# Optimization experiments

Measured on AMD Instinct MI355X. Metric: run time of the kernel, lower is better.

## Reference

```python
import jax, jax.numpy as jnp
import numpy as np

B, T = 32, 128
D_PATCH, D_PLM, H, P = 128, 768, 4, 64
HD = D_PLM // H          # head_dim = 192
N_TOK = 15               # 1+1+4+4+4+1 patch tokens
EPS = 1e-5


def layernorm(x, g, b):
    m = jnp.mean(x, axis=-1, keepdims=True)
    v = jnp.var(x, axis=-1, keepdims=True)
    return (x - m) * jax.lax.rsqrt(v + EPS) * g + b


def setup_inputs() -> dict:
    key = jax.random.key(0)
    ks = jax.random.split(key, 12)
    nrm = lambda k, shp, s: jax.random.normal(k, shp, jnp.float32) * s
    return {
        "state":    jax.random.normal(ks[0], (B, T, 6, 6), jnp.float32),
        # per-feature patch embedders: scalar feats (0,1,5) in_dim=1, windowed feats (2,3,4) in_dim=3
        "w_scalar": nrm(ks[1], (3, 1, D_PATCH), 0.5),
        "b_scalar": jnp.zeros((3, D_PATCH), jnp.float32),
        "w_patch":  nrm(ks[2], (3, 3, D_PATCH), 0.3),
        "b_patch":  jnp.zeros((3, D_PATCH), jnp.float32),
        "feat_emb": nrm(ks[3], (6, D_PATCH), 0.02),
        "pn_g": jnp.ones((D_PATCH,), jnp.float32),
        "pn_b": jnp.zeros((D_PATCH,), jnp.float32),
        "wq": nrm(ks[4], (D_PATCH, D_PLM), 0.05), "bq": jnp.zeros((D_PLM,), jnp.float32),
        "wk": nrm(ks[5], (D_PLM, D_PLM), 0.02),   "bk": jnp.zeros((D_PLM,), jnp.float32),
        "wv": nrm(ks[6], (D_PLM, D_PLM), 0.02),   "bv": jnp.zeros((D_PLM,), jnp.float32),
        "wp": nrm(ks[7], (D_PATCH, D_PLM), 0.05), "bp": jnp.zeros((D_PLM,), jnp.float32),
        "wo": nrm(ks[8], (D_PLM, D_PLM), 0.02),   "bo": jnp.zeros((D_PLM,), jnp.float32),
        "on_g": jnp.ones((D_PLM,), jnp.float32),
        "on_b": jnp.zeros((D_PLM,), jnp.float32),
        # text prototype bank (rows sampled from word embedding table in the original)
        "protos": nrm(ks[9], (P, D_PLM), 1.0),
    }


def reference(state, w_scalar, b_scalar, w_patch, b_patch, feat_emb, pn_g, pn_b,
              wq, bq, wk, bk, wv, bv, wp, bp, wo, bo, on_g, on_b, protos):
    b, t = state.shape[0], state.shape[1]
    s = state.reshape(b * t, 6, 6)                       # (N,6,6)
    N = s.shape[0]

    # scalar features 0,1,5: last timestep, patch_size=1 -> 1 token each
    sc = s[:, jnp.array([0, 1, 5]), -1]                  # (N,3)
    sc_emb = sc[..., None] * w_scalar[:, 0][None] + b_scalar[None]   # (N,3,Dp)
    sc_emb = sc_emb + feat_emb[jnp.array([0, 1, 5])][None]

    # windowed features 2,3,4: length 6, patch_len 3, stride 1 -> 4 tokens each
    pf = s[:, jnp.array([2, 3, 4]), :]                   # (N,3,6)
    win = jnp.stack([pf[..., i:i + 3] for i in range(4)], axis=2)    # (N,3,4,3)
    p_emb = jnp.einsum('nfkp,fpd->nfkd', win, w_patch) + b_patch[None, :, None]
    p_emb = p_emb + feat_emb[jnp.array([2, 3, 4])][None, :, None]

    # concat in feature order 0,1,2,3,4,5 -> (N,15,Dp), then LayerNorm
    pe = jnp.concatenate([sc_emb[:, 0:1], sc_emb[:, 1:2],
                          p_emb[:, 0], p_emb[:, 1], p_emb[:, 2],
                          sc_emb[:, 2:3]], axis=1)
    pe = layernorm(pe, pn_g, pn_b)

    # cross-attention: Q from patches, K/V from 64 text prototypes
    q = (pe @ wq + bq).reshape(N, N_TOK, H, HD)
    k = (protos @ wk + bk).reshape(P, H, HD)
    v = (protos @ wv + bv).reshape(P, H, HD)
    scores = jnp.einsum('nthd,phd->nhtp', q, k) / np.float32(np.sqrt(HD))
    attn = jax.nn.softmax(scores, axis=-1)               # (N,H,T,P)
    rep = jnp.einsum('nhtp,phd->nthd', attn, v).reshape(N, N_TOK, D_PLM)

    out = (rep @ wo + bo) + (pe @ wp + bp)               # dual projection residual
    out = layernorm(out, on_g, on_b)
    return out.reshape(b, t, N_TOK, D_PLM)
```

## Files before the change

### kernel.cpp

```cpp
#include <hip/hip_runtime.h>

#define NTOK 15
#define DP   128
#define DM   768
#define NH   4
#define HD   192
#define NP   64
#define EPSF 1e-5f
#define RPB  4
#define TPB  512
#define KW   384

typedef __attribute__((ext_vector_type(8))) short bf16x8;
typedef __attribute__((ext_vector_type(4))) float f32x4;

__device__ __forceinline__ unsigned short f2bf(float x) {
    unsigned u = __float_as_uint(x);
    u = (u + 0x7FFF + ((u >> 16) & 1)) >> 16;
    return (unsigned short)u;
}
__device__ __forceinline__ int swzP(int row, int b) { return row * 256 + (b ^ ((row & 7) << 4)); }
__device__ __forceinline__ int swzB(int row, int b) { return row * 512 + (b ^ ((row & 7) << 4)); }

__global__ __launch_bounds__(768) void kv_kernel(
    const float* __restrict__ protos,
    const float* __restrict__ wk, const float* __restrict__ bk,
    const float* __restrict__ wv, const float* __restrict__ bv,
    float* __restrict__ Kraw, float* __restrict__ Vf)
{
    int r = blockIdx.x;
    int j = threadIdx.x;
    __shared__ float prow[DM];
    prow[j] = protos[r * DM + j];
    __syncthreads();
    float aK = bk[j], aV = bv[j];
    for (int d = 0; d < DM; ++d) {
        float p = prow[d];
        aK += p * wk[d * DM + j];
        aV += p * wv[d * DM + j];
    }
    int h = j / HD, jj = j - h * HD;
    Kraw[(h * NP + r) * HD + jj] = aK;
    Vf[r * DM + j] = aV;
}

__global__ __launch_bounds__(256) void fold_kernel(
    const float* __restrict__ Kraw, const float* __restrict__ Vf,
    const float* __restrict__ wq, const float* __restrict__ bq,
    const float* __restrict__ wo, const float* __restrict__ wp,
    unsigned short* __restrict__ KWb, float* __restrict__ kqb,
    unsigned short* __restrict__ Wcat)
{
    int b = blockIdx.x, tid = threadIdx.x;
    if (b >= 256) {
        int idx = (b - 256) * 256 + tid;
        int j = idx >> 7, d = idx & 127;
        Wcat[(size_t)j * KW + 256 + d] = f2bf(wp[d * DM + j]);
        return;
    }
    int hp = b, h = hp >> 6, p = hp & 63;
    __shared__ float Kl[HD], Vl[HD];
    if (tid < HD) {
        Kl[tid] = Kraw[hp * HD + tid];
        Vl[tid] = Vf[p * DM + h * HD + tid];
    }
    __syncthreads();
    const float scale = 0.07216878364870323f;
    if (tid < DP) {
        float a = 0.f;
        for (int l = 0; l < HD; ++l) a += wq[tid * DM + h * HD + l] * Kl[l];
        KWb[hp * DP + tid] = f2bf(scale * a);
    } else if (tid == DP) {
        float a = 0.f;
        for (int l = 0; l < HD; ++l) a += bq[h * HD + l] * Kl[l];
        kqb[hp] = scale * a;
    }
    for (int jj = 0; jj < 3; ++jj) {
        int j = jj * 256 + tid;
        float a = 0.f;
        for (int l = 0; l < HD; ++l) a += wo[(h * HD + l) * DM + j] * Vl[l];
        Wcat[(size_t)j * KW + hp] = f2bf(a);
    }
}

__global__ __launch_bounds__(TPB, 4) void row_kernel(
    const float* __restrict__ state,
    const float* __restrict__ w_scalar, const float* __restrict__ b_scalar,
    const float* __restrict__ w_patch,  const float* __restrict__ b_patch,
    const float* __restrict__ feat_emb,
    const float* __restrict__ pn_g, const float* __restrict__ pn_b,
    const unsigned short* __restrict__ KWb, const float* __restrict__ kqb,
    const unsigned short* __restrict__ Wcat,
    const float* __restrict__ bp, const float* __restrict__ bo,
    const float* __restrict__ on_g, const float* __restrict__ on_b,
    float* __restrict__ out, int Nrows)
{
    int tid = threadIdx.x;
    int w = tid >> 6, lane = tid & 63;
    int kg = lane >> 4, lr = lane & 15;
    int nb = blockIdx.x;

    __shared__ __align__(16) char bufA[64 * 512];
    __shared__ __align__(16) char pebf[64 * 256];
    __shared__ float srow[RPB * 36];
    __shared__ float redS[8][64], redS2[8][64];

    float* peF = (float*)bufA;

    if (tid < RPB * 36) {
        int rr = tid / 36;
        int gr = nb * RPB + rr;
        srow[tid] = (gr < Nrows) ? state[(size_t)gr * 36 + (tid - rr * 36)] : 0.f;
    }
    __syncthreads();

    for (int idx = tid; idx < RPB * NTOK * DP; idx += TPB) {
        int rr  = idx / (NTOK * DP);
        int rem = idx - rr * (NTOK * DP);
        int t = rem >> 7, d = rem & 127;
        const float* sr = &srow[rr * 36];
        float val;
        if (t == 0) {
            val = sr[5]  * w_scalar[0 * DP + d] + b_scalar[0 * DP + d] + feat_emb[0 * DP + d];
        } else if (t == 1) {
            val = sr[11] * w_scalar[1 * DP + d] + b_scalar[1 * DP + d] + feat_emb[1 * DP + d];
        } else if (t == 14) {
            val = sr[35] * w_scalar[2 * DP + d] + b_scalar[2 * DP + d] + feat_emb[5 * DP + d];
        } else {
            int f = (t - 2) / 4;
            int k = (t - 2) % 4;
            const float* pr = &sr[(2 + f) * 6];
            float acc = b_patch[f * DP + d] + feat_emb[(2 + f) * DP + d];
            for (int p = 0; p < 3; ++p) acc += pr[k + p] * w_patch[(f * 3 + p) * DP + d];
            val = acc;
        }
        peF[(rr * 16 + t) * DP + d] = val;
    }
    __syncthreads();

    const int h = w >> 1;
    bf16x8 ka[4][4];
    float4 kqv[4];
    {
        const unsigned short* kwh = KWb + (size_t)h * NP * DP;
        #pragma unroll
        for (int Mt = 0; Mt < 4; ++Mt) {
            #pragma unroll
            for (int kk = 0; kk < 4; ++kk)
                ka[Mt][kk] = *(const bf16x8*)(kwh + (Mt * 16 + lr) * DP + kk * 32 + kg * 8);
            kqv[Mt] = *(const float4*)(kqb + h * 64 + Mt * 16 + kg * 4);
        }
    }

    {
        int g = tid >> 3, ln = tid & 7;
        int t = g & 15;
        int gr = nb * RPB + (g >> 4);
        if (t == 15 || gr >= Nrows) {
            for (int d = ln; d < DP; d += 8)
                *(unsigned short*)(pebf + swzP(g, d * 2)) = 0;
        } else {
            float s = 0.f, s2 = 0.f;
            for (int d = ln; d < DP; d += 8) { float x = peF[g * DP + d]; s += x; s2 += x * x; }
            for (int off = 4; off; off >>= 1) {
                s  += __shfl_xor(s,  off, 64);
                s2 += __shfl_xor(s2, off, 64);
            }
            float m   = s / DP;
            float var = s2 / DP - m * m;
            float rin = 1.0f / sqrtf(var + EPSF);
            for (int d = ln; d < DP; d += 8) {
                float x = (peF[g * DP + d] - m) * rin * pn_g[d] + pn_b[d];
                *(unsigned short*)(pebf + swzP(g, d * 2)) = f2bf(x);
            }
        }
    }
    __syncthreads();

    {
        int Nt0 = (w & 1) * 2;
        #pragma unroll
        for (int Ntl = 0; Ntl < 2; ++Ntl) {
            int Nt = Nt0 + Ntl;
            bf16x8 qb[4];
            #pragma unroll
            for (int kk = 0; kk < 4; ++kk)
                qb[kk] = *(const bf16x8*)(pebf + swzP(Nt * 16 + lr, (kk * 32 + kg * 8) * 2));
            f32x4 sacc[4];
            #pragma unroll
            for (int Mt = 0; Mt < 4; ++Mt) sacc[Mt] = (f32x4){0.f, 0.f, 0.f, 0.f};
            #pragma unroll
            for (int kk = 0; kk < 4; ++kk)
                #pragma unroll
                for (int Mt = 0; Mt < 4; ++Mt)
                    sacc[Mt] = __builtin_amdgcn_mfma_f32_16x16x32_bf16(ka[Mt][kk], qb[kk], sacc[Mt], 0, 0, 0);
            #pragma unroll
            for (int Mt = 0; Mt < 4; ++Mt) {
                sacc[Mt][0] += kqv[Mt].x; sacc[Mt][1] += kqv[Mt].y;
                sacc[Mt][2] += kqv[Mt].z; sacc[Mt][3] += kqv[Mt].w;
            }
            float mx = -3.4e38f;
            #pragma unroll
            for (int Mt = 0; Mt < 4; ++Mt)
                #pragma unroll
                for (int r = 0; r < 4; ++r) mx = fmaxf(mx, sacc[Mt][r]);
            mx = fmaxf(mx, __shfl_xor(mx, 16, 64));
            mx = fmaxf(mx, __shfl_xor(mx, 32, 64));
            float sum = 0.f;
            f32x4 ee[4];
            #pragma unroll
            for (int Mt = 0; Mt < 4; ++Mt)
                #pragma unroll
                for (int r = 0; r < 4; ++r) { float e = __expf(sacc[Mt][r] - mx); ee[Mt][r] = e; sum += e; }
            sum += __shfl_xor(sum, 16, 64);
            sum += __shfl_xor(sum, 32, 64);
            float inv = 1.0f / sum;
            #pragma unroll
            for (int Mt = 0; Mt < 4; ++Mt)
                #pragma unroll
                for (int r = 0; r < 4; ++r) {
                    int c = h * 64 + Mt * 16 + kg * 4 + r;
                    *(unsigned short*)(bufA + swzB(Nt * 16 + lr, c * 2)) = f2bf(ee[Mt][r] * inv);
                }
        }
    }
    __syncthreads();

    const int n0 = w * 96;
    const unsigned short* wptr[6];
    #pragma unroll
    for (int nt = 0; nt < 6; ++nt)
        wptr[nt] = Wcat + (size_t)(n0 + nt * 16 + lr) * KW + kg * 8;

    #pragma unroll
    for (int half = 0; half < 2; ++half) {
        f32x4 acc[6][2];
        #pragma unroll
        for (int nt = 0; nt < 6; ++nt) {
            int col = n0 + nt * 16 + lr;
            float bias = bo[col] + bp[col];
            acc[nt][0] = (f32x4){bias, bias, bias, bias};
            acc[nt][1] = (f32x4){bias, bias, bias, bias};
        }
        bf16x8 b0[6], b1[6];
        #pragma unroll
        for (int nt = 0; nt < 6; ++nt) b0[nt] = *(const bf16x8*)(wptr[nt]);
        #pragma unroll
        for (int kkc = 0; kkc < 3; ++kkc) {
            #pragma unroll
            for (int kk = 0; kk < 4; ++kk) {
                const int ks = kkc * 4 + kk;
                bf16x8 aw0, aw1;
                if (kkc < 2) {
                    aw0 = *(const bf16x8*)(bufA + swzB((half * 2 + 0) * 16 + lr, (kkc * 128 + kk * 32 + kg * 8) * 2));
                    aw1 = *(const bf16x8*)(bufA + swzB((half * 2 + 1) * 16 + lr, (kkc * 128 + kk * 32 + kg * 8) * 2));
                } else {
                    aw0 = *(const bf16x8*)(pebf + swzP((half * 2 + 0) * 16 + lr, (kk * 32 + kg * 8) * 2));
                    aw1 = *(const bf16x8*)(pebf + swzP((half * 2 + 1) * 16 + lr, (kk * 32 + kg * 8) * 2));
                }
                if (ks + 1 < 12) {
                    if ((ks & 1) == 0) {
                        #pragma unroll
                        for (int nt = 0; nt < 6; ++nt)
                            b1[nt] = *(const bf16x8*)(wptr[nt] + (ks + 1) * 32);
                    } else {
                        #pragma unroll
                        for (int nt = 0; nt < 6; ++nt)
                            b0[nt] = *(const bf16x8*)(wptr[nt] + (ks + 1) * 32);
                    }
                }
                if ((ks & 1) == 0) {
                    #pragma unroll
                    for (int nt = 0; nt < 6; ++nt) {
                        acc[nt][0] = __builtin_amdgcn_mfma_f32_16x16x32_bf16(aw0, b0[nt], acc[nt][0], 0, 0, 0);
                        acc[nt][1] = __builtin_amdgcn_mfma_f32_16x16x32_bf16(aw1, b0[nt], acc[nt][1], 0, 0, 0);
                    }
                } else {
                    #pragma unroll
                    for (int nt = 0; nt < 6; ++nt) {
                        acc[nt][0] = __builtin_amdgcn_mfma_f32_16x16x32_bf16(aw0, b1[nt], acc[nt][0], 0, 0, 0);
                        acc[nt][1] = __builtin_amdgcn_mfma_f32_16x16x32_bf16(aw1, b1[nt], acc[nt][1], 0, 0, 0);
                    }
                }
            }
        }
        #pragma unroll
        for (int Mtl = 0; Mtl < 2; ++Mtl)
            #pragma unroll
            for (int r = 0; r < 4; ++r) {
                float s = 0.f, q = 0.f;
                #pragma unroll
                for (int nt = 0; nt < 6; ++nt) { float v = acc[nt][Mtl][r]; s += v; q += v * v; }
                #pragma unroll
                for (int off = 8; off; off >>= 1) {
                    s += __shfl_xor(s, off, 64);
                    q += __shfl_xor(q, off, 64);
                }
                if (lr == 0) {
                    int tok = (half * 2 + Mtl) * 16 + kg * 4 + r;
                    redS [w][tok] = s;
                    redS2[w][tok] = q;
                }
            }
        __syncthreads();
        #pragma unroll
        for (int Mtl = 0; Mtl < 2; ++Mtl) {
            float mA[4], riA[4];
            #pragma unroll
            for (int r = 0; r < 4; ++r) {
                int tok = (half * 2 + Mtl) * 16 + kg * 4 + r;
                float ts = 0.f, tq = 0.f;
                #pragma unroll
                for (int ww = 0; ww < 8; ++ww) { ts += redS[ww][tok]; tq += redS2[ww][tok]; }
                float mm  = ts / DM;
                float var = tq / DM - mm * mm;
                mA[r]  = mm;
                riA[r] = 1.0f / sqrtf(var + EPSF);
            }
            #pragma unroll
            for (int nt = 0; nt < 6; ++nt) {
                int col = n0 + nt * 16 + lr;
                float g = on_g[col], bb = on_b[col];
                #pragma unroll
                for (int r = 0; r < 4; ++r) {
                    int tok = (half * 2 + Mtl) * 16 + kg * 4 + r;
                    int t = tok & 15, rr = tok >> 4;
                    int gr = nb * RPB + rr;
                    if (t < NTOK && gr < Nrows)
                        out[((size_t)gr * NTOK + t) * DM + col] =
                            (acc[nt][Mtl][r] - mA[r]) * riA[r] * g + bb;
                }
            }
        }
    }
}

extern "C" void kernel_launch(void* const* d_in, const int* in_sizes, int n_in,
                              void* d_out, int out_size, void* d_ws, size_t ws_size,
                              hipStream_t stream) {
    const float* state    = (const float*)d_in[0];
    const float* w_scalar = (const float*)d_in[1];
    const float* b_scalar = (const float*)d_in[2];
    const float* w_patch  = (const float*)d_in[3];
    const float* b_patch  = (const float*)d_in[4];
    const float* feat_emb = (const float*)d_in[5];
    const float* pn_g     = (const float*)d_in[6];
    const float* pn_b     = (const float*)d_in[7];
    const float* wq       = (const float*)d_in[8];
    const float* bq       = (const float*)d_in[9];
    const float* wk       = (const float*)d_in[10];
    const float* bk       = (const float*)d_in[11];
    const float* wv       = (const float*)d_in[12];
    const float* bv       = (const float*)d_in[13];
    const float* wp       = (const float*)d_in[14];
    const float* bp       = (const float*)d_in[15];
    const float* wo       = (const float*)d_in[16];
    const float* bo       = (const float*)d_in[17];
    const float* on_g     = (const float*)d_in[18];
    const float* on_b     = (const float*)d_in[19];
    const float* protos   = (const float*)d_in[20];
    float* out = (float*)d_out;

    float*          Kraw = (float*)d_ws;
    float*          Vf   = Kraw + 256 * HD;
    float*          kqbp = Vf + NP * DM;
    unsigned short* KWb  = (unsigned short*)(kqbp + 256);
    unsigned short* Wcat = KWb + 256 * DP;

    int N = in_sizes[0] / 36;
    int nblk = (N + RPB - 1) / RPB;

    hipLaunchKernelGGL(kv_kernel, dim3(NP), dim3(DM), 0, stream,
                       protos, wk, bk, wv, bv, Kraw, Vf);
    hipLaunchKernelGGL(fold_kernel, dim3(640), dim3(256), 0, stream,
                       Kraw, Vf, wq, bq, wo, wp, KWb, kqbp, Wcat);
    hipLaunchKernelGGL(row_kernel, dim3(nblk), dim3(TPB), 0, stream,
                       state, w_scalar, b_scalar, w_patch, b_patch, feat_emb,
                       pn_g, pn_b, KWb, kqbp, Wcat, bp, bo, on_g, on_b,
                       out, N);
}
```

Before: 310.2 us.

## Split fused row kernel into attention phase and projection phase via workspace buffer

Splits the fused per-row kernel into two kernels. The first computes patch embedding, layernorm and the softmax attention weights, then writes a bf16 concatenated A matrix to workspace. The second runs the dual-projection GEMM plus output layernorm, staging results in LDS so stores are coalesced float4 writes. It also spreads kv_kernel over more, smaller blocks and drops the software double-buffering of weight loads in the fallback path. The gain in occupancy and write coalescing is paid for with an extra global round trip of the intermediate activations, and the new path only runs if the workspace is large enough.

```diff
diff --git a/kernel.cpp b/kernel.cpp
--- a/kernel.cpp
+++ b/kernel.cpp
@@ -7,12 +7,11 @@
 #define HD   192
 #define NP   64
 #define EPSF 1e-5f
-#define RPB  4
-#define TPB  512
-#define KW   384
+#define KW2  384
 
 typedef __attribute__((ext_vector_type(8))) short bf16x8;
 typedef __attribute__((ext_vector_type(4))) float f32x4;
+typedef __attribute__((ext_vector_type(4))) unsigned short us4;
 
 __device__ __forceinline__ unsigned short f2bf(float x) {
     unsigned u = __float_as_uint(x);
@@ -22,16 +21,17 @@
 __device__ __forceinline__ int swzP(int row, int b) { return row * 256 + (b ^ ((row & 7) << 4)); }
 __device__ __forceinline__ int swzB(int row, int b) { return row * 512 + (b ^ ((row & 7) << 4)); }
 
-__global__ __launch_bounds__(768) void kv_kernel(
+__global__ __launch_bounds__(192) void kv_kernel(
     const float* __restrict__ protos,
     const float* __restrict__ wk, const float* __restrict__ bk,
     const float* __restrict__ wv, const float* __restrict__ bv,
     float* __restrict__ Kraw, float* __restrict__ Vf)
 {
-    int r = blockIdx.x;
-    int j = threadIdx.x;
+    int r  = blockIdx.x >> 2;
+    int jc = blockIdx.x & 3;
+    int j  = jc * 192 + threadIdx.x;
     __shared__ float prow[DM];
-    prow[j] = protos[r * DM + j];
+    for (int i = threadIdx.x; i < DM; i += 192) prow[i] = protos[r * DM + i];
     __syncthreads();
     float aK = bk[j], aV = bv[j];
     for (int d = 0; d < DM; ++d) {
@@ -55,7 +55,7 @@
     if (b >= 256) {
         int idx = (b - 256) * 256 + tid;
         int j = idx >> 7, d = idx & 127;
-        Wcat[(size_t)j * KW + 256 + d] = f2bf(wp[d * DM + j]);
+        Wcat[(size_t)j * KW2 + 256 + d] = f2bf(wp[d * DM + j]);
         return;
     }
     int hp = b, h = hp >> 6, p = hp & 63;
@@ -79,11 +79,257 @@
         int j = jj * 256 + tid;
         float a = 0.f;
         for (int l = 0; l < HD; ++l) a += wo[(h * HD + l) * DM + j] * Vl[l];
-        Wcat[(size_t)j * KW + hp] = f2bf(a);
+        Wcat[(size_t)j * KW2 + hp] = f2bf(a);
     }
 }
 
-__global__ __launch_bounds__(TPB, 4) void row_kernel(
+__global__ __launch_bounds__(256, 4) void phaseA_kernel(
+    const float* __restrict__ state,
+    const float* __restrict__ w_scalar, const float* __restrict__ b_scalar,
+    const float* __restrict__ w_patch,  const float* __restrict__ b_patch,
+    const float* __restrict__ feat_emb,
+    const float* __restrict__ pn_g, const float* __restrict__ pn_b,
+    const unsigned short* __restrict__ KWb, const float* __restrict__ kqb,
+    unsigned short* __restrict__ abufG, int Nrows)
+{
+    int tid = threadIdx.x;
+    int w = tid >> 6, lane = tid & 63;
+    int kg = lane >> 4, lr = lane & 15;
+    int nb = blockIdx.x;
+    size_t rowbase = (size_t)nb * 32;
+
+    __shared__ float peF[32 * DP];
+    __shared__ __align__(16) char pebf[32 * 256];
+    __shared__ float srow[72];
+
+    if (tid < 72) {
+        int rr = tid / 36;
+        int gr = nb * 2 + rr;
+        srow[tid] = (gr < Nrows) ? state[(size_t)gr * 36 + (tid - rr * 36)] : 0.f;
+    }
+    __syncthreads();
+
+    #pragma unroll
+    for (int it = 0; it < 16; ++it) {
+        int idx = it * 256 + tid;
+        int row = idx >> 7, d = idx & 127;
+        int t = row & 15;
+        const float* sr = &srow[(row >> 4) * 36];
+        float val;
+        if (t == 15) {
+            val = 0.f;
+        } else if (t == 0) {
+            val = sr[5]  * w_scalar[0 * DP + d] + b_scalar[0 * DP + d] + feat_emb[0 * DP + d];
+        } else if (t == 1) {
+            val = sr[11] * w_scalar[1 * DP + d] + b_scalar[1 * DP + d] + feat_emb[1 * DP + d];
+        } else if (t == 14) {
+            val = sr[35] * w_scalar[2 * DP + d] + b_scalar[2 * DP + d] + feat_emb[5 * DP + d];
+        } else {
+            int f = (t - 2) / 4;
+            int k = (t - 2) % 4;
+            const float* pr = &sr[(2 + f) * 6];
+            float acc = b_patch[f * DP + d] + feat_emb[(2 + f) * DP + d];
+            for (int p = 0; p < 3; ++p) acc += pr[k + p] * w_patch[(f * 3 + p) * DP + d];
+            val = acc;
+        }
+        peF[row * DP + d] = val;
+    }
+    __syncthreads();
+
+    {
+        int g = tid >> 3, ln = tid & 7;
+        int t = g & 15;
+        int gr = nb * 2 + (g >> 4);
+        if (t == 15 || gr >= Nrows) {
+            for (int d = ln; d < DP; d += 8)
+                *(unsigned short*)(pebf + swzP(g, d * 2)) = 0;
+        } else {
+            float s = 0.f, s2 = 0.f;
+            for (int d = ln; d < DP; d += 8) { float x = peF[g * DP + d]; s += x; s2 += x * x; }
+            for (int off = 4; off; off >>= 1) {
+                s  += __shfl_xor(s,  off, 64);
+                s2 += __shfl_xor(s2, off, 64);
+            }
+            float m   = s / DP;
+            float var = s2 / DP - m * m;
+            float rin = 1.0f / sqrtf(var + EPSF);
+            for (int d = ln; d < DP; d += 8) {
+                float x = (peF[g * DP + d] - m) * rin * pn_g[d] + pn_b[d];
+                *(unsigned short*)(pebf + swzP(g, d * 2)) = f2bf(x);
+            }
+        }
+    }
+    __syncthreads();
+
+    {
+        const int h = w;
+        const unsigned short* kwh = KWb + (size_t)h * NP * DP;
+        bf16x8 ka[4][4];
+        float4 kqv[4];
+        #pragma unroll
+        for (int Mt = 0; Mt < 4; ++Mt) {
+            #pragma unroll
+            for (int kk = 0; kk < 4; ++kk)
+                ka[Mt][kk] = *(const bf16x8*)(kwh + (Mt * 16 + lr) * DP + kk * 32 + kg * 8);
+            kqv[Mt] = *(const float4*)(kqb + h * 64 + Mt * 16 + kg * 4);
+        }
+        #pragma unroll
+        for (int Ntl = 0; Ntl < 2; ++Ntl) {
+            bf16x8 qb[4];
+            #pragma unroll
+            for (int kk = 0; kk < 4; ++kk)
+                qb[kk] = *(const bf16x8*)(pebf + swzP(Ntl * 16 + lr, (kk * 32 + kg * 8) * 2));
+            f32x4 sacc[4];
+            #pragma unroll
+            for (int Mt = 0; Mt < 4; ++Mt) sacc[Mt] = (f32x4){0.f, 0.f, 0.f, 0.f};
+            #pragma unroll
+            for (int kk = 0; kk < 4; ++kk)
+                #pragma unroll
+                for (int Mt = 0; Mt < 4; ++Mt)
+                    sacc[Mt] = __builtin_amdgcn_mfma_f32_16x16x32_bf16(ka[Mt][kk], qb[kk], sacc[Mt], 0, 0, 0);
+            #pragma unroll
+            for (int Mt = 0; Mt < 4; ++Mt) {
+                sacc[Mt][0] += kqv[Mt].x; sacc[Mt][1] += kqv[Mt].y;
+                sacc[Mt][2] += kqv[Mt].z; sacc[Mt][3] += kqv[Mt].w;
+            }
+            float mx = -3.4e38f;
+            #pragma unroll
+            for (int Mt = 0; Mt < 4; ++Mt)
+                #pragma unroll
+                for (int r = 0; r < 4; ++r) mx = fmaxf(mx, sacc[Mt][r]);
+            mx = fmaxf(mx, __shfl_xor(mx, 16, 64));
+            mx = fmaxf(mx, __shfl_xor(mx, 32, 64));
+            float sum = 0.f;
+            f32x4 ee[4];
+            #pragma unroll
+            for (int Mt = 0; Mt < 4; ++Mt)
+                #pragma unroll
+                for (int r = 0; r < 4; ++r) { float e = __expf(sacc[Mt][r] - mx); ee[Mt][r] = e; sum += e; }
+            sum += __shfl_xor(sum, 16, 64);
+            sum += __shfl_xor(sum, 32, 64);
+            float inv = 1.0f / sum;
+            unsigned short* dst = abufG + (rowbase + Ntl * 16 + lr) * KW2 + h * 64 + kg * 4;
+            #pragma unroll
+            for (int Mt = 0; Mt < 4; ++Mt) {
+                us4 v = { f2bf(ee[Mt][0] * inv), f2bf(ee[Mt][1] * inv),
+                          f2bf(ee[Mt][2] * inv), f2bf(ee[Mt][3] * inv) };
+                *(us4*)(dst + Mt * 16) = v;
+            }
+        }
+    }
+
+    #pragma unroll
+    for (int c = 0; c < 2; ++c) {
+        int idx = c * 256 + tid;
+        int row = idx >> 4, chunk = idx & 15;
+        bf16x8 v = *(const bf16x8*)(pebf + swzP(row, chunk * 16));
+        *(bf16x8*)(abufG + (rowbase + row) * KW2 + 256 + chunk * 8) = v;
+    }
+}
+
+__global__ __launch_bounds__(512, 2) void phaseB_kernel(
+    const unsigned short* __restrict__ abufG,
+    const unsigned short* __restrict__ Wcat,
+    const float* __restrict__ bp, const float* __restrict__ bo,
+    const float* __restrict__ on_g, const float* __restrict__ on_b,
+    float* __restrict__ out, int Nrows)
+{
+    int tid = threadIdx.x;
+    int w = tid >> 6, lane = tid & 63;
+    int kg = lane >> 4, lr = lane & 15;
+    int nb = blockIdx.x;
+    const int n0 = w * 96;
+
+    __shared__ __align__(16) float stage[16 * 772];
+    __shared__ float redS[8][64], redS2[8][64];
+
+    const unsigned short* aptr = abufG + (size_t)nb * 64 * KW2;
+
+    float gcol[6], bcol[6];
+    f32x4 acc[6][4];
+    #pragma unroll
+    for (int nt = 0; nt < 6; ++nt) {
+        int col = n0 + nt * 16 + lr;
+        gcol[nt] = on_g[col]; bcol[nt] = on_b[col];
+        float bias = bo[col] + bp[col];
+        #pragma unroll
+        for (int Mt = 0; Mt < 4; ++Mt) acc[nt][Mt] = (f32x4){bias, bias, bias, bias};
+    }
+
+    #pragma unroll
+    for (int ks = 0; ks < 12; ++ks) {
+        bf16x8 aw[4];
+        #pragma unroll
+        for (int Mt = 0; Mt < 4; ++Mt)
+            aw[Mt] = *(const bf16x8*)(aptr + (Mt * 16 + lr) * KW2 + ks * 32 + kg * 8);
+        #pragma unroll
+        for (int nt = 0; nt < 6; ++nt) {
+            bf16x8 b = *(const bf16x8*)(Wcat + (size_t)(n0 + nt * 16 + lr) * KW2 + ks * 32 + kg * 8);
+            #pragma unroll
+            for (int Mt = 0; Mt < 4; ++Mt)
+                acc[nt][Mt] = __builtin_amdgcn_mfma_f32_16x16x32_bf16(aw[Mt], b, acc[nt][Mt], 0, 0, 0);
+        }
+    }
+
+    #pragma unroll
+    for (int Mt = 0; Mt < 4; ++Mt)
+        #pragma unroll
+        for (int r = 0; r < 4; ++r) {
+            float s = 0.f, q = 0.f;
+            #pragma unroll
+            for (int nt = 0; nt < 6; ++nt) { float v = acc[nt][Mt][r]; s += v; q += v * v; }
+            #pragma unroll
+            for (int off = 8; off; off >>= 1) {
+                s += __shfl_xor(s, off, 64);
+                q += __shfl_xor(q, off, 64);
+            }
+            if (lr == 0) {
+                int tok = Mt * 16 + kg * 4 + r;
+                redS [w][tok] = s;
+                redS2[w][tok] = q;
+            }
+        }
+    __syncthreads();
+    float mA[4][4], riA[4][4];
+    #pragma unroll
+    for (int Mt = 0; Mt < 4; ++Mt)
+        #pragma unroll
+        for (int r = 0; r < 4; ++r) {
+            int tok = Mt * 16 + kg * 4 + r;
+            float ts = 0.f, tq = 0.f;
+            #pragma unroll
+            for (int ww = 0; ww < 8; ++ww) { ts += redS[ww][tok]; tq += redS2[ww][tok]; }
+            float mm  = ts / DM;
+            float var = tq / DM - mm * mm;
+            mA[Mt][r]  = mm;
+            riA[Mt][r] = 1.0f / sqrtf(var + EPSF);
+        }
+
+    #pragma unroll
+    for (int Mt = 0; Mt < 4; ++Mt) {
+        __syncthreads();
+        #pragma unroll
+        for (int nt = 0; nt < 6; ++nt)
+            #pragma unroll
+            for (int r = 0; r < 4; ++r)
+                stage[(kg * 4 + r) * 772 + n0 + nt * 16 + lr] =
+                    (acc[nt][Mt][r] - mA[Mt][r]) * riA[Mt][r] * gcol[nt] + bcol[nt];
+        __syncthreads();
+        int gr = nb * 4 + Mt;
+        if (gr < Nrows) {
+            #pragma unroll
+            for (int v = 0; v < 6; ++v) {
+                int f = v * 512 + tid;
+                int row = f / 192, c4 = f - row * 192;
+                if (row < NTOK)
+                    *(float4*)(out + ((size_t)gr * NTOK + row) * DM + c4 * 4) =
+                        *(const float4*)(&stage[row * 772 + c4 * 4]);
+            }
+        }
+    }
+}
+
+__global__ __launch_bounds__(512, 4) void row_fused_kernel(
     const float* __restrict__ state,
     const float* __restrict__ w_scalar, const float* __restrict__ b_scalar,
     const float* __restrict__ w_patch,  const float* __restrict__ b_patch,
@@ -102,19 +348,19 @@
 
     __shared__ __align__(16) char bufA[64 * 512];
     __shared__ __align__(16) char pebf[64 * 256];
-    __shared__ float srow[RPB * 36];
+    __shared__ float srow[4 * 36];
     __shared__ float redS[8][64], redS2[8][64];
 
     float* peF = (float*)bufA;
 
-    if (tid < RPB * 36) {
+    if (tid < 4 * 36) {
         int rr = tid / 36;
-        int gr = nb * RPB + rr;
+        int gr = nb * 4 + rr;
         srow[tid] = (gr < Nrows) ? state[(size_t)gr * 36 + (tid - rr * 36)] : 0.f;
     }
     __syncthreads();
 
-    for (int idx = tid; idx < RPB * NTOK * DP; idx += TPB) {
+    for (int idx = tid; idx < 4 * NTOK * DP; idx += 512) {
         int rr  = idx / (NTOK * DP);
         int rem = idx - rr * (NTOK * DP);
         int t = rem >> 7, d = rem & 127;
@@ -155,7 +401,7 @@
     {
         int g = tid >> 3, ln = tid & 7;
         int t = g & 15;
-        int gr = nb * RPB + (g >> 4);
+        int gr = nb * 4 + (g >> 4);
         if (t == 15 || gr >= Nrows) {
             for (int d = ln; d < DP; d += 8)
                 *(unsigned short*)(pebf + swzP(g, d * 2)) = 0;
@@ -227,11 +473,6 @@
     __syncthreads();
 
     const int n0 = w * 96;
-    const unsigned short* wptr[6];
-    #pragma unroll
-    for (int nt = 0; nt < 6; ++nt)
-        wptr[nt] = Wcat + (size_t)(n0 + nt * 16 + lr) * KW + kg * 8;
-
     #pragma unroll
     for (int half = 0; half < 2; ++half) {
         f32x4 acc[6][2];
@@ -242,14 +483,10 @@
             acc[nt][0] = (f32x4){bias, bias, bias, bias};
             acc[nt][1] = (f32x4){bias, bias, bias, bias};
         }
-        bf16x8 b0[6], b1[6];
-        #pragma unroll
-        for (int nt = 0; nt < 6; ++nt) b0[nt] = *(const bf16x8*)(wptr[nt]);
         #pragma unroll
         for (int kkc = 0; kkc < 3; ++kkc) {
             #pragma unroll
             for (int kk = 0; kk < 4; ++kk) {
-                const int ks = kkc * 4 + kk;
                 bf16x8 aw0, aw1;
                 if (kkc < 2) {
                     aw0 = *(const bf16x8*)(bufA + swzB((half * 2 + 0) * 16 + lr, (kkc * 128 + kk * 32 + kg * 8) * 2));
@@ -258,29 +495,12 @@
                     aw0 = *(const bf16x8*)(pebf + swzP((half * 2 + 0) * 16 + lr, (kk * 32 + kg * 8) * 2));
                     aw1 = *(const bf16x8*)(pebf + swzP((half * 2 + 1) * 16 + lr, (kk * 32 + kg * 8) * 2));
                 }
-                if (ks + 1 < 12) {
-                    if ((ks & 1) == 0) {
-                        #pragma unroll
-                        for (int nt = 0; nt < 6; ++nt)
-                            b1[nt] = *(const bf16x8*)(wptr[nt] + (ks + 1) * 32);
-                    } else {
-                        #pragma unroll
-                        for (int nt = 0; nt < 6; ++nt)
-                            b0[nt] = *(const bf16x8*)(wptr[nt] + (ks + 1) * 32);
-                    }
-                }
-                if ((ks & 1) == 0) {
-                    #pragma unroll
-                    for (int nt = 0; nt < 6; ++nt) {
-                        acc[nt][0] = __builtin_amdgcn_mfma_f32_16x16x32_bf16(aw0, b0[nt], acc[nt][0], 0, 0, 0);
-                        acc[nt][1] = __builtin_amdgcn_mfma_f32_16x16x32_bf16(aw1, b0[nt], acc[nt][1], 0, 0, 0);
-                    }
-                } else {
-                    #pragma unroll
-                    for (int nt = 0; nt < 6; ++nt) {
-                        acc[nt][0] = __builtin_amdgcn_mfma_f32_16x16x32_bf16(aw0, b1[nt], acc[nt][0], 0, 0, 0);
-                        acc[nt][1] = __builtin_amdgcn_mfma_f32_16x16x32_bf16(aw1, b1[nt], acc[nt][1], 0, 0, 0);
-                    }
+                int ks = kkc * 4 + kk;
+                #pragma unroll
+                for (int nt = 0; nt < 6; ++nt) {
+                    bf16x8 b = *(const bf16x8*)(Wcat + (size_t)(n0 + nt * 16 + lr) * KW2 + ks * 32 + kg * 8);
+                    acc[nt][0] = __builtin_amdgcn_mfma_f32_16x16x32_bf16(aw0, b, acc[nt][0], 0, 0, 0);
+                    acc[nt][1] = __builtin_amdgcn_mfma_f32_16x16x32_bf16(aw1, b, acc[nt][1], 0, 0, 0);
                 }
             }
         }
@@ -325,7 +545,7 @@
                 for (int r = 0; r < 4; ++r) {
                     int tok = (half * 2 + Mtl) * 16 + kg * 4 + r;
                     int t = tok & 15, rr = tok >> 4;
-                    int gr = nb * RPB + rr;
+                    int gr = nb * 4 + rr;
                     if (t < NTOK && gr < Nrows)
                         out[((size_t)gr * NTOK + t) * DM + col] =
                             (acc[nt][Mtl][r] - mA[r]) * riA[r] * g + bb;
@@ -366,16 +586,29 @@
     float*          kqbp = Vf + NP * DM;
     unsigned short* KWb  = (unsigned short*)(kqbp + 256);
     unsigned short* Wcat = KWb + 256 * DP;
+    unsigned short* abufG = Wcat + (size_t)DM * KW2;
 
     int N = in_sizes[0] / 36;
-    int nblk = (N + RPB - 1) / RPB;
-
-    hipLaunchKernelGGL(kv_kernel, dim3(NP), dim3(DM), 0, stream,
+    int nblkA = (N + 1) / 2;
+    int nblkB = (N + 3) / 4;
+    size_t tokrows = (size_t)nblkB * 64;
+    size_t need = 1049600ull + tokrows * KW2 * 2ull;
+
+    hipLaunchKernelGGL(kv_kernel, dim3(256), dim3(192), 0, stream,
                        protos, wk, bk, wv, bv, Kraw, Vf);
     hipLaunchKernelGGL(fold_kernel, dim3(640), dim3(256), 0, stream,
                        Kraw, Vf, wq, bq, wo, wp, KWb, kqbp, Wcat);
-    hipLaunchKernelGGL(row_kernel, dim3(nblk), dim3(TPB), 0, stream,
-                       state, w_scalar, b_scalar, w_patch, b_patch, feat_emb,
-                       pn_g, pn_b, KWb, kqbp, Wcat, bp, bo, on_g, on_b,
-                       out, N);
+
+    if (ws_size >= need) {
+        hipLaunchKernelGGL(phaseA_kernel, dim3(nblkA), dim3(256), 0, stream,
+                           state, w_scalar, b_scalar, w_patch, b_patch, feat_emb,
+                           pn_g, pn_b, KWb, kqbp, abufG, N);
+        hipLaunchKernelGGL(phaseB_kernel, dim3(nblkB), dim3(512), 0, stream,
+                           abufG, Wcat, bp, bo, on_g, on_b, out, N);
+    } else {
+        hipLaunchKernelGGL(row_fused_kernel, dim3(nblkB), dim3(512), 0, stream,
+                           state, w_scalar, b_scalar, w_patch, b_patch, feat_emb,
+                           pn_g, pn_b, KWb, kqbp, Wcat, bp, bo, on_g, on_b,
+                           out, N);
+    }
 }
```

Result: faster. 297.1 us (-4.2%).

## Split row kernel into attention and projection phases via global bf16 buffer

Applied to the files above, without the earlier changes.

Fuses the K/V projection into the fold kernel, which removes one launch but recomputes K and V per head-prototype block. Splits the fused row kernel in two. Phase A does embedding, LayerNorm and attention for 2 rows per 256-thread block and writes the bf16 [attn|pe] activations to a workspace buffer. Phase B runs the combined output projection GEMM plus LayerNorm on 64-token tiles and stages results in LDS for coalesced float4 stores. This trades an extra global round-trip of activations for simpler, better-occupied kernels, and the phase kernels are skipped entirely if the workspace is too small.

```diff
diff --git a/kernel.cpp b/kernel.cpp
--- a/kernel.cpp
+++ b/kernel.cpp
@@ -7,12 +7,12 @@
 #define HD   192
 #define NP   64
 #define EPSF 1e-5f
-#define RPB  4
-#define TPB  512
-#define KW   384
+#define KW2  384
+#define ABSTR 528
 
 typedef __attribute__((ext_vector_type(8))) short bf16x8;
 typedef __attribute__((ext_vector_type(4))) float f32x4;
+typedef __attribute__((ext_vector_type(4))) unsigned short us4;
 
 __device__ __forceinline__ unsigned short f2bf(float x) {
     unsigned u = __float_as_uint(x);
@@ -22,30 +22,10 @@
 __device__ __forceinline__ int swzP(int row, int b) { return row * 256 + (b ^ ((row & 7) << 4)); }
 __device__ __forceinline__ int swzB(int row, int b) { return row * 512 + (b ^ ((row & 7) << 4)); }
 
-__global__ __launch_bounds__(768) void kv_kernel(
+__global__ __launch_bounds__(256) void fold_kernel(
     const float* __restrict__ protos,
     const float* __restrict__ wk, const float* __restrict__ bk,
     const float* __restrict__ wv, const float* __restrict__ bv,
-    float* __restrict__ Kraw, float* __restrict__ Vf)
-{
-    int r = blockIdx.x;
-    int j = threadIdx.x;
-    __shared__ float prow[DM];
-    prow[j] = protos[r * DM + j];
-    __syncthreads();
-    float aK = bk[j], aV = bv[j];
-    for (int d = 0; d < DM; ++d) {
-        float p = prow[d];
-        aK += p * wk[d * DM + j];
-        aV += p * wv[d * DM + j];
-    }
-    int h = j / HD, jj = j - h * HD;
-    Kraw[(h * NP + r) * HD + jj] = aK;
-    Vf[r * DM + j] = aV;
-}
-
-__global__ __launch_bounds__(256) void fold_kernel(
-    const float* __restrict__ Kraw, const float* __restrict__ Vf,
     const float* __restrict__ wq, const float* __restrict__ bq,
     const float* __restrict__ wo, const float* __restrict__ wp,
     unsigned short* __restrict__ KWb, float* __restrict__ kqb,
@@ -55,14 +35,23 @@
     if (b >= 256) {
         int idx = (b - 256) * 256 + tid;
         int j = idx >> 7, d = idx & 127;
-        Wcat[(size_t)j * KW + 256 + d] = f2bf(wp[d * DM + j]);
+        Wcat[(size_t)j * KW2 + 256 + d] = f2bf(wp[d * DM + j]);
         return;
     }
     int hp = b, h = hp >> 6, p = hp & 63;
+    __shared__ float prow[DM];
     __shared__ float Kl[HD], Vl[HD];
+    for (int i = tid; i < DM; i += 256) prow[i] = protos[p * DM + i];
+    __syncthreads();
     if (tid < HD) {
-        Kl[tid] = Kraw[hp * HD + tid];
-        Vl[tid] = Vf[p * DM + h * HD + tid];
+        float aK = bk[h * HD + tid], aV = bv[h * HD + tid];
+        for (int e = 0; e < DM; ++e) {
+            float pr = prow[e];
+            aK += pr * wk[e * DM + h * HD + tid];
+            aV += pr * wv[e * DM + h * HD + tid];
+        }
+        Kl[tid] = aK;
+        Vl[tid] = aV;
     }
     __syncthreads();
     const float scale = 0.07216878364870323f;
@@ -79,48 +68,48 @@
         int j = jj * 256 + tid;
         float a = 0.f;
         for (int l = 0; l < HD; ++l) a += wo[(h * HD + l) * DM + j] * Vl[l];
-        Wcat[(size_t)j * KW + hp] = f2bf(a);
-    }
-}
-
-__global__ __launch_bounds__(TPB, 4) void row_kernel(
+        Wcat[(size_t)j * KW2 + hp] = f2bf(a);
+    }
+}
+
+__global__ __launch_bounds__(256, 4) void phaseA_kernel(
     const float* __restrict__ state,
     const float* __restrict__ w_scalar, const float* __restrict__ b_scalar,
     const float* __restrict__ w_patch,  const float* __restrict__ b_patch,
     const float* __restrict__ feat_emb,
     const float* __restrict__ pn_g, const float* __restrict__ pn_b,
     const unsigned short* __restrict__ KWb, const float* __restrict__ kqb,
-    const unsigned short* __restrict__ Wcat,
-    const float* __restrict__ bp, const float* __restrict__ bo,
-    const float* __restrict__ on_g, const float* __restrict__ on_b,
-    float* __restrict__ out, int Nrows)
+    unsigned short* __restrict__ abufG, int Nrows)
 {
     int tid = threadIdx.x;
     int w = tid >> 6, lane = tid & 63;
     int kg = lane >> 4, lr = lane & 15;
     int nb = blockIdx.x;
-
-    __shared__ __align__(16) char bufA[64 * 512];
-    __shared__ __align__(16) char pebf[64 * 256];
-    __shared__ float srow[RPB * 36];
-    __shared__ float redS[8][64], redS2[8][64];
-
-    float* peF = (float*)bufA;
-
-    if (tid < RPB * 36) {
+    size_t rowbase = (size_t)nb * 32;
+
+    __shared__ __align__(16) char buf0[32 * ABSTR];
+    __shared__ __align__(16) char pebf[32 * 256];
+    __shared__ float srow[72];
+
+    float* peF = (float*)buf0;
+
+    if (tid < 72) {
         int rr = tid / 36;
-        int gr = nb * RPB + rr;
+        int gr = nb * 2 + rr;
         srow[tid] = (gr < Nrows) ? state[(size_t)gr * 36 + (tid - rr * 36)] : 0.f;
     }
     __syncthreads();
 
-    for (int idx = tid; idx < RPB * NTOK * DP; idx += TPB) {
-        int rr  = idx / (NTOK * DP);
-        int rem = idx - rr * (NTOK * DP);
-        int t = rem >> 7, d = rem & 127;
-        const float* sr = &srow[rr * 36];
+    #pragma unroll
+    for (int it = 0; it < 16; ++it) {
+        int idx = it * 256 + tid;
+        int row = idx >> 7, d = idx & 127;
+        int t = row & 15;
+        const float* sr = &srow[(row >> 4) * 36];
         float val;
-        if (t == 0) {
+        if (t == 15) {
+            val = 0.f;
+        } else if (t == 0) {
             val = sr[5]  * w_scalar[0 * DP + d] + b_scalar[0 * DP + d] + feat_emb[0 * DP + d];
         } else if (t == 1) {
             val = sr[11] * w_scalar[1 * DP + d] + b_scalar[1 * DP + d] + feat_emb[1 * DP + d];
@@ -134,28 +123,14 @@
             for (int p = 0; p < 3; ++p) acc += pr[k + p] * w_patch[(f * 3 + p) * DP + d];
             val = acc;
         }
-        peF[(rr * 16 + t) * DP + d] = val;
-    }
-    __syncthreads();
-
-    const int h = w >> 1;
-    bf16x8 ka[4][4];
-    float4 kqv[4];
-    {
-        const unsigned short* kwh = KWb + (size_t)h * NP * DP;
-        #pragma unroll
-        for (int Mt = 0; Mt < 4; ++Mt) {
-            #pragma unroll
-            for (int kk = 0; kk < 4; ++kk)
-                ka[Mt][kk] = *(const bf16x8*)(kwh + (Mt * 16 + lr) * DP + kk * 32 + kg * 8);
-            kqv[Mt] = *(const float4*)(kqb + h * 64 + Mt * 16 + kg * 4);
-        }
-    }
+        peF[row * DP + d] = val;
+    }
+    __syncthreads();
 
     {
         int g = tid >> 3, ln = tid & 7;
         int t = g & 15;
-        int gr = nb * RPB + (g >> 4);
+        int gr = nb * 2 + (g >> 4);
         if (t == 15 || gr >= Nrows) {
             for (int d = ln; d < DP; d += 8)
                 *(unsigned short*)(pebf + swzP(g, d * 2)) = 0;
@@ -178,14 +153,23 @@
     __syncthreads();
 
     {
-        int Nt0 = (w & 1) * 2;
+        const int h = w;
+        const unsigned short* kwh = KWb + (size_t)h * NP * DP;
+        bf16x8 ka[4][4];
+        float4 kqv[4];
+        #pragma unroll
+        for (int Mt = 0; Mt < 4; ++Mt) {
+            #pragma unroll
+            for (int kk = 0; kk < 4; ++kk)
+                ka[Mt][kk] = *(const bf16x8*)(kwh + (Mt * 16 + lr) * DP + kk * 32 + kg * 8);
+            kqv[Mt] = *(const float4*)(kqb + h * 64 + Mt * 16 + kg * 4);
+        }
         #pragma unroll
         for (int Ntl = 0; Ntl < 2; ++Ntl) {
-            int Nt = Nt0 + Ntl;
             bf16x8 qb[4];
             #pragma unroll
             for (int kk = 0; kk < 4; ++kk)
-                qb[kk] = *(const bf16x8*)(pebf + swzP(Nt * 16 + lr, (kk * 32 + kg * 8) * 2));
+                qb[kk] = *(const bf16x8*)(pebf + swzP(Ntl * 16 + lr, (kk * 32 + kg * 8) * 2));
             f32x4 sacc[4];
             #pragma unroll
             for (int Mt = 0; Mt < 4; ++Mt) sacc[Mt] = (f32x4){0.f, 0.f, 0.f, 0.f};
@@ -215,121 +199,127 @@
             sum += __shfl_xor(sum, 16, 64);
             sum += __shfl_xor(sum, 32, 64);
             float inv = 1.0f / sum;
+            int row = Ntl * 16 + lr;
+            #pragma unroll
+            for (int Mt = 0; Mt < 4; ++Mt) {
+                us4 v = { f2bf(ee[Mt][0] * inv), f2bf(ee[Mt][1] * inv),
+                          f2bf(ee[Mt][2] * inv), f2bf(ee[Mt][3] * inv) };
+                *(us4*)(buf0 + row * ABSTR + (h * 64 + Mt * 16 + kg * 4) * 2) = v;
+            }
+        }
+    }
+    __syncthreads();
+
+    #pragma unroll
+    for (int c = 0; c < 6; ++c) {
+        int idx = c * 256 + tid;
+        int row = idx / 48, chunk = idx % 48;
+        bf16x8 v;
+        if (chunk < 32) v = *(const bf16x8*)(buf0 + row * ABSTR + chunk * 16);
+        else            v = *(const bf16x8*)(pebf + swzP(row, (chunk - 32) * 16));
+        *(bf16x8*)(abufG + (rowbase + row) * KW2 + chunk * 8) = v;
+    }
+}
+
+__global__ __launch_bounds__(512, 2) void phaseB_kernel(
+    const unsigned short* __restrict__ abufG,
+    const unsigned short* __restrict__ Wcat,
+    const float* __restrict__ bp, const float* __restrict__ bo,
+    const float* __restrict__ on_g, const float* __restrict__ on_b,
+    float* __restrict__ out, int Nrows)
+{
+    int tid = threadIdx.x;
+    int w = tid >> 6, lane = tid & 63;
+    int kg = lane >> 4, lr = lane & 15;
+    int nb = blockIdx.x;
+    const int n0 = w * 96;
+
+    __shared__ __align__(16) float stage[16 * 772];
+    __shared__ float redS[8][64], redS2[8][64];
+
+    const unsigned short* aptr = abufG + (size_t)nb * 64 * KW2;
+
+    float gcol[6], bcol[6];
+    f32x4 acc[6][4];
+    #pragma unroll
+    for (int nt = 0; nt < 6; ++nt) {
+        int col = n0 + nt * 16 + lr;
+        gcol[nt] = on_g[col]; bcol[nt] = on_b[col];
+        float bias = bo[col] + bp[col];
+        #pragma unroll
+        for (int Mt = 0; Mt < 4; ++Mt) acc[nt][Mt] = (f32x4){bias, bias, bias, bias};
+    }
+
+    #pragma unroll
+    for (int ks = 0; ks < 12; ++ks) {
+        bf16x8 aw[4];
+        #pragma unroll
+        for (int Mt = 0; Mt < 4; ++Mt)
+            aw[Mt] = *(const bf16x8*)(aptr + (Mt * 16 + lr) * KW2 + ks * 32 + kg * 8);
+        __builtin_amdgcn_s_setprio(1);
+        #pragma unroll
+        for (int nt = 0; nt < 6; ++nt) {
+            bf16x8 b = *(const bf16x8*)(Wcat + (size_t)(n0 + nt * 16 + lr) * KW2 + ks * 32 + kg * 8);
             #pragma unroll
             for (int Mt = 0; Mt < 4; ++Mt)
-                #pragma unroll
-                for (int r = 0; r < 4; ++r) {
-                    int c = h * 64 + Mt * 16 + kg * 4 + r;
-                    *(unsigned short*)(bufA + swzB(Nt * 16 + lr, c * 2)) = f2bf(ee[Mt][r] * inv);
-                }
-        }
-    }
-    __syncthreads();
-
-    const int n0 = w * 96;
-    const unsigned short* wptr[6];
-    #pragma unroll
-    for (int nt = 0; nt < 6; ++nt)
-        wptr[nt] = Wcat + (size_t)(n0 + nt * 16 + lr) * KW + kg * 8;
-
-    #pragma unroll
-    for (int half = 0; half < 2; ++half) {
-        f32x4 acc[6][2];
-        #pragma unroll
-        for (int nt = 0; nt < 6; ++nt) {
-            int col = n0 + nt * 16 + lr;
-            float bias = bo[col] + bp[col];
-            acc[nt][0] = (f32x4){bias, bias, bias, bias};
-            acc[nt][1] = (f32x4){bias, bias, bias, bias};
-        }
-        bf16x8 b0[6], b1[6];
-        #pragma unroll
-        for (int nt = 0; nt < 6; ++nt) b0[nt] = *(const bf16x8*)(wptr[nt]);
-        #pragma unroll
-        for (int kkc = 0; kkc < 3; ++kkc) {
-            #pragma unroll
-            for (int kk = 0; kk < 4; ++kk) {
-                const int ks = kkc * 4 + kk;
-                bf16x8 aw0, aw1;
-                if (kkc < 2) {
-                    aw0 = *(const bf16x8*)(bufA + swzB((half * 2 + 0) * 16 + lr, (kkc * 128 + kk * 32 + kg * 8) * 2));
-                    aw1 = *(const bf16x8*)(bufA + swzB((half * 2 + 1) * 16 + lr, (kkc * 128 + kk * 32 + kg * 8) * 2));
-                } else {
-                    aw0 = *(const bf16x8*)(pebf + swzP((half * 2 + 0) * 16 + lr, (kk * 32 + kg * 8) * 2));
-                    aw1 = *(const bf16x8*)(pebf + swzP((half * 2 + 1) * 16 + lr, (kk * 32 + kg * 8) * 2));
-                }
-                if (ks + 1 < 12) {
-                    if ((ks & 1) == 0) {
-                        #pragma unroll
-                        for (int nt = 0; nt < 6; ++nt)
-                            b1[nt] = *(const bf16x8*)(wptr[nt] + (ks + 1) * 32);
-                    } else {
-                        #pragma unroll
-                        for (int nt = 0; nt < 6; ++nt)
-                            b0[nt] = *(const bf16x8*)(wptr[nt] + (ks + 1) * 32);
-                    }
-                }
-                if ((ks & 1) == 0) {
-                    #pragma unroll
-                    for (int nt = 0; nt < 6; ++nt) {
-                        acc[nt][0] = __builtin_amdgcn_mfma_f32_16x16x32_bf16(aw0, b0[nt], acc[nt][0], 0, 0, 0);
-                        acc[nt][1] = __builtin_amdgcn_mfma_f32_16x16x32_bf16(aw1, b0[nt], acc[nt][1], 0, 0, 0);
-                    }
-                } else {
-                    #pragma unroll
-                    for (int nt = 0; nt < 6; ++nt) {
-                        acc[nt][0] = __builtin_amdgcn_mfma_f32_16x16x32_bf16(aw0, b1[nt], acc[nt][0], 0, 0, 0);
-                        acc[nt][1] = __builtin_amdgcn_mfma_f32_16x16x32_bf16(aw1, b1[nt], acc[nt][1], 0, 0, 0);
-                    }
-                }
-            }
-        }
-        #pragma unroll
-        for (int Mtl = 0; Mtl < 2; ++Mtl)
-            #pragma unroll
-            for (int r = 0; r < 4; ++r) {
-                float s = 0.f, q = 0.f;
-                #pragma unroll
-                for (int nt = 0; nt < 6; ++nt) { float v = acc[nt][Mtl][r]; s += v; q += v * v; }
-                #pragma unroll
-                for (int off = 8; off; off >>= 1) {
-                    s += __shfl_xor(s, off, 64);
-                    q += __shfl_xor(q, off, 64);
-                }
-                if (lr == 0) {
-                    int tok = (half * 2 + Mtl) * 16 + kg * 4 + r;
-                    redS [w][tok] = s;
-                    redS2[w][tok] = q;
-                }
-            }
+                acc[nt][Mt] = __builtin_amdgcn_mfma_f32_16x16x32_bf16(aw[Mt], b, acc[nt][Mt], 0, 0, 0);
+        }
+        __builtin_amdgcn_s_setprio(0);
+    }
+
+    #pragma unroll
+    for (int Mt = 0; Mt < 4; ++Mt)
+        #pragma unroll
+        for (int r = 0; r < 4; ++r) {
+            float s = 0.f, q = 0.f;
+            #pragma unroll
+            for (int nt = 0; nt < 6; ++nt) { float v = acc[nt][Mt][r]; s += v; q += v * v; }
+            #pragma unroll
+            for (int off = 8; off; off >>= 1) {
+                s += __shfl_xor(s, off, 64);
+                q += __shfl_xor(q, off, 64);
+            }
+            if (lr == 0) {
+                int tok = Mt * 16 + kg * 4 + r;
+                redS [w][tok] = s;
+                redS2[w][tok] = q;
+            }
+        }
+    __syncthreads();
+    float mA[4][4], riA[4][4];
+    #pragma unroll
+    for (int Mt = 0; Mt < 4; ++Mt)
+        #pragma unroll
+        for (int r = 0; r < 4; ++r) {
+            int tok = Mt * 16 + kg * 4 + r;
+            float ts = 0.f, tq = 0.f;
+            #pragma unroll
+            for (int ww = 0; ww < 8; ++ww) { ts += redS[ww][tok]; tq += redS2[ww][tok]; }
+            float mm  = ts / DM;
+            float var = tq / DM - mm * mm;
+            mA[Mt][r]  = mm;
+            riA[Mt][r] = 1.0f / sqrtf(var + EPSF);
+        }
+
+    #pragma unroll
+    for (int Mt = 0; Mt < 4; ++Mt) {
         __syncthreads();
         #pragma unroll
-        for (int Mtl = 0; Mtl < 2; ++Mtl) {
-            float mA[4], riA[4];
-            #pragma unroll
-            for (int r = 0; r < 4; ++r) {
-                int tok = (half * 2 + Mtl) * 16 + kg * 4 + r;
-                float ts = 0.f, tq = 0.f;
-                #pragma unroll
-                for (int ww = 0; ww < 8; ++ww) { ts += redS[ww][tok]; tq += redS2[ww][tok]; }
-                float mm  = ts / DM;
-                float var = tq / DM - mm * mm;
-                mA[r]  = mm;
-                riA[r] = 1.0f / sqrtf(var + EPSF);
-            }
-            #pragma unroll
-            for (int nt = 0; nt < 6; ++nt) {
-                int col = n0 + nt * 16 + lr;
-                float g = on_g[col], bb = on_b[col];
-                #pragma unroll
-                for (int r = 0; r < 4; ++r) {
-                    int tok = (half * 2 + Mtl) * 16 + kg * 4 + r;
-                    int t = tok & 15, rr = tok >> 4;
-                    int gr = nb * RPB + rr;
-                    if (t < NTOK && gr < Nrows)
-                        out[((size_t)gr * NTOK + t) * DM + col] =
-                            (acc[nt][Mtl][r] - mA[r]) * riA[r] * g + bb;
-                }
+        for (int nt = 0; nt < 6; ++nt)
+            #pragma unroll
+            for (int r = 0; r < 4; ++r)
+                stage[(kg * 4 + r) * 772 + n0 + nt * 16 + lr] =
+                    (acc[nt][Mt][r] - mA[Mt][r]) * riA[Mt][r] * gcol[nt] + bcol[nt];
+        __syncthreads();
+        int gr = nb * 4 + Mt;
+        if (gr < Nrows) {
+            #pragma unroll
+            for (int v = 0; v < 6; ++v) {
+                int f = v * 512 + tid;
+                int row = f / 192, c4 = f - row * 192;
+                if (row < NTOK)
+                    *(float4*)(out + ((size_t)gr * NTOK + row) * DM + c4 * 4) =
+                        *(const float4*)(&stage[row * 772 + c4 * 4]);
             }
         }
     }
@@ -361,21 +351,25 @@
     const float* protos   = (const float*)d_in[20];
     float* out = (float*)d_out;
 
-    float*          Kraw = (float*)d_ws;
-    float*          Vf   = Kraw + 256 * HD;
-    float*          kqbp = Vf + NP * DM;
-    unsigned short* KWb  = (unsigned short*)(kqbp + 256);
-    unsigned short* Wcat = KWb + 256 * DP;
+    float*          kqbp  = (float*)d_ws;
+    unsigned short* KWb   = (unsigned short*)(kqbp + 256);
+    unsigned short* Wcat  = KWb + 256 * DP;
+    unsigned short* abufG = Wcat + (size_t)DM * KW2;
 
     int N = in_sizes[0] / 36;
-    int nblk = (N + RPB - 1) / RPB;
-
-    hipLaunchKernelGGL(kv_kernel, dim3(NP), dim3(DM), 0, stream,
-                       protos, wk, bk, wv, bv, Kraw, Vf);
+    int nblkA = (N + 1) / 2;
+    int nblkB = (N + 3) / 4;
+    size_t tokrows = (size_t)nblkB * 64;
+    size_t need = 1024ull + 65536ull + 589824ull + tokrows * KW2 * 2ull;
+
     hipLaunchKernelGGL(fold_kernel, dim3(640), dim3(256), 0, stream,
-                       Kraw, Vf, wq, bq, wo, wp, KWb, kqbp, Wcat);
-    hipLaunchKernelGGL(row_kernel, dim3(nblk), dim3(TPB), 0, stream,
-                       state, w_scalar, b_scalar, w_patch, b_patch, feat_emb,
-                       pn_g, pn_b, KWb, kqbp, Wcat, bp, bo, on_g, on_b,
-                       out, N);
-}
+                       protos, wk, bk, wv, bv, wq, bq, wo, wp,
+                       KWb, kqbp, Wcat);
+    if (ws_size >= need) {
+        hipLaunchKernelGGL(phaseA_kernel, dim3(nblkA), dim3(256), 0, stream,
+                           state, w_scalar, b_scalar, w_patch, b_patch, feat_emb,
+                           pn_g, pn_b, KWb, kqbp, abufG, N);
+        hipLaunchKernelGGL(phaseB_kernel, dim3(nblkB), dim3(512), 0, stream,
+                           abufG, Wcat, bp, bo, on_g, on_b, out, N);
+    }
+}
```

After: 265.1 us. 1.17x faster.
